# Kernel optimization log

Measured on AMD Instinct MI355X. Metric: run time of the kernel, lower is better.

The kernel has to match this reference:

```python
import jax, jax.numpy as jnp
import numpy as np

H, D, BS = 32, 128, 16  # num heads, head dim, paged-KV block size
ROPE_BASE = 10000.0
NEG_INF = -1e30


def setup_inputs() -> dict:
    key = jax.random.key(0)
    ks = jax.random.split(key, 8)
    B, KV, hidden = 8, 2048, H * D  # decode: one new token per sequence
    max_blocks = KV // BS
    num_slots = B * KV

    hidden_states = jax.random.normal(ks[0], (B, hidden), jnp.float32) * 0.02

    # rotary cos/sin for the current position of each sequence (pos = KV-1)
    inv_freq = 1.0 / (ROPE_BASE ** (jnp.arange(0, D, 2, dtype=jnp.float32) / D))
    pos = jnp.full((B,), KV - 1, jnp.float32)
    ang = pos[:, None] * inv_freq[None, :]            # [B, D/2]
    cos, sin = jnp.cos(ang), jnp.sin(ang)

    w_qkv = jax.random.normal(ks[1], (3 * H * D, hidden), jnp.float32) * 0.02
    b_qkv = jax.random.normal(ks[2], (3 * H * D,), jnp.float32) * 0.02
    w_o = jax.random.normal(ks[3], (hidden, H * D), jnp.float32) * 0.02

    k_cache = jax.random.normal(ks[4], (num_slots, H, D), jnp.float32) * 0.5
    v_cache = jax.random.normal(ks[5], (num_slots, H, D), jnp.float32) * 0.5

    # contiguous block allocation: seq b owns blocks [b*max_blocks, (b+1)*max_blocks)
    block_tables = jnp.arange(B * max_blocks, dtype=jnp.int32).reshape(B, max_blocks)
    slots = (jnp.arange(B, dtype=jnp.int32) * KV + (KV - 1)).astype(jnp.int32)
    input_lengths = jnp.full((B,), KV, jnp.int32)

    return dict(hidden_states=hidden_states, cos=cos, sin=sin,
                w_qkv=w_qkv, b_qkv=b_qkv, w_o=w_o,
                k_cache=k_cache, v_cache=v_cache,
                block_tables=block_tables, slots=slots,
                input_lengths=input_lengths, max_s=KV)


def _rope(x, cos, sin):
    # flash-attn style (non-interleaved) rotary: split head dim in halves
    x1, x2 = jnp.split(x, 2, axis=-1)                 # [T, H, D/2] each
    c, s = cos[:, None, :], sin[:, None, :]
    return jnp.concatenate([x1 * c - x2 * s, x1 * s + x2 * c], axis=-1)


def reference(hidden_states, cos, sin, w_qkv, b_qkv, w_o,
              k_cache, v_cache, block_tables, slots, input_lengths, max_s):
    B = hidden_states.shape[0]
    # fused QKV projection (c_attn, bias=True)
    qkv = hidden_states @ w_qkv.T + b_qkv             # [B, 3*H*D]
    q, k, v = jnp.split(qkv, 3, axis=1)
    q = q.reshape(B, H, D)
    k = k.reshape(B, H, D)
    v = v.reshape(B, H, D)

    # rotary applied in-place to q and k[:,0] in the original
    q = _rope(q, cos, sin)
    k = _rope(k, cos, sin)

    # reshape_and_cache: scatter current k/v into the paged KV cache
    k_cache = k_cache.at[slots].set(k)
    v_cache = v_cache.at[slots].set(v)

    # paged_attn: gather KV via block tables, masked softmax over valid length
    pos = jnp.arange(max_s)                           # [S]
    idx = block_tables[:, pos // BS] * BS + (pos % BS)[None, :]  # [B, S] slot ids
    keys = k_cache[idx]                               # [B, S, H, D]
    vals = v_cache[idx]                               # [B, S, H, D]

    scale = D ** -0.5
    scores = jnp.einsum('bhd,bshd->bhs', q, keys) * scale
    valid = pos[None, :] < input_lengths[:, None]     # [B, S]
    scores = jnp.where(valid[:, None, :], scores, NEG_INF)
    probs = jax.nn.softmax(scores, axis=-1)
    attn = jnp.einsum('bhs,bshd->bhd', probs, vals)   # [B, H, D]

    # o_proj (c_proj, bias=False)
    return attn.reshape(B, H * D) @ w_o.T
```

## Files before the change

kernel.cpp:

```cpp
#include <hip/hip_runtime.h>

#define NH 32
#define HD 128
#define PBS 16
#define HIDDEN (NH * HD)
#define QKVN (3 * HIDDEN)
#define NSPLIT 8
#define KC 512

template <int NR>
__global__ __launch_bounds__(256) void gemv_lds(const float* __restrict__ x,
                                                const float* __restrict__ W,
                                                const float* __restrict__ bias,
                                                float* __restrict__ out,
                                                int N, int K) {
    __shared__ float xs[8][KC];
    const int tid  = threadIdx.x;
    const int lane = tid & 63;
    const int wid  = tid >> 6;
    const int n0   = blockIdx.x * (NR * 4) + wid * NR;
    const float* w0 = W + (size_t)n0 * K;

    float acc[NR][8];
#pragma unroll
    for (int r = 0; r < NR; ++r)
#pragma unroll
        for (int b = 0; b < 8; ++b) acc[r][b] = 0.f;

    for (int kc = 0; kc < K; kc += KC) {
        __syncthreads();
        {
            const int bq  = tid >> 5;
            const int t32 = tid & 31;
            const float* xb = x + (size_t)bq * K + kc;
#pragma unroll
            for (int j = 0; j < 4; ++j) {
                const int off = (t32 + j * 32) * 4;
                *reinterpret_cast<float4*>(&xs[bq][off]) =
                    *reinterpret_cast<const float4*>(xb + off);
            }
        }
        __syncthreads();
#pragma unroll
        for (int j = 0; j < 2; ++j) {
            const int kk = lane * 4 + j * 256;
            float4 w4[NR];
#pragma unroll
            for (int r = 0; r < NR; ++r)
                w4[r] = *reinterpret_cast<const float4*>(w0 + (size_t)r * K + kc + kk);
#pragma unroll
            for (int b = 0; b < 8; ++b) {
                const float4 x4 = *reinterpret_cast<const float4*>(&xs[b][kk]);
#pragma unroll
                for (int r = 0; r < NR; ++r)
                    acc[r][b] += w4[r].x * x4.x + w4[r].y * x4.y +
                                 w4[r].z * x4.z + w4[r].w * x4.w;
            }
        }
    }
#pragma unroll
    for (int r = 0; r < NR; ++r)
#pragma unroll
        for (int b = 0; b < 8; ++b)
#pragma unroll
            for (int off = 32; off > 0; off >>= 1)
                acc[r][b] += __shfl_xor(acc[r][b], off, 64);
    if (lane == 0) {
#pragma unroll
        for (int r = 0; r < NR; ++r) {
            const float bv = bias ? bias[n0 + r] : 0.f;
#pragma unroll
            for (int b = 0; b < 8; ++b)
                out[(size_t)b * N + n0 + r] = acc[r][b] + bv;
        }
    }
}

__global__ __launch_bounds__(256) void rope_k(float* __restrict__ qkv,
                                              const float* __restrict__ cosb,
                                              const float* __restrict__ sinb,
                                              int B) {
    const int tid = blockIdx.x * blockDim.x + threadIdx.x;
    const int total = 2 * B * NH * (HD / 2);
    if (tid >= total) return;
    const int d = tid % (HD / 2);
    const int h = (tid / (HD / 2)) % NH;
    const int b = (tid / (HD / 2) / NH) % B;
    const int part = tid / (HD / 2) / NH / B;
    const float c = cosb[b * (HD / 2) + d];
    const float s = sinb[b * (HD / 2) + d];
    float* p = qkv + (size_t)b * QKVN + part * HIDDEN + h * HD + d;
    const float x1 = p[0];
    const float x2 = p[HD / 2];
    p[0]      = x1 * c - x2 * s;
    p[HD / 2] = x1 * s + x2 * c;
}

__global__ __launch_bounds__(256) void attn_part(const float* __restrict__ qkv,
                                                 const float* __restrict__ k_cache,
                                                 const float* __restrict__ v_cache,
                                                 const int* __restrict__ block_tables,
                                                 const int* __restrict__ slots,
                                                 const int* __restrict__ lengths,
                                                 float* __restrict__ part_o,
                                                 float* __restrict__ part_ml,
                                                 int S, int max_blocks) {
    const int split = blockIdx.x % NSPLIT;
    const int bh    = blockIdx.x / NSPLIT;
    const int b     = bh >> 5;
    const int h     = bh & 31;
    const int SP    = S / NSPLIT;
    const int base  = split * SP;

    __shared__ int   bt[64];
    __shared__ float stage[4][HD + 2];

    const int tid  = threadIdx.x;
    const int lane = tid & 63;
    const int wid  = tid >> 6;
    const int nw   = 4;
    const int half = lane >> 5;
    const int l32  = lane & 31;

    const int nbt = SP / PBS;
    for (int i = tid; i < nbt; i += blockDim.x)
        bt[i] = block_tables[b * max_blocks + base / PBS + i];
    __syncthreads();

    const int slot_b = slots[b];
    const int len    = lengths[b];
    const float scale = 0.088388347648318447f;

    const float* qp   = qkv + (size_t)b * QKVN + h * HD;
    const float* newk = qp + HIDDEN;
    const float* newv = qp + 2 * HIDDEN;
    const float4 q4 = *reinterpret_cast<const float4*>(qp + l32 * 4);

    float m = -1e30f, l = 0.f;
    float4 acc[8];
#pragma unroll
    for (int u = 0; u < 8; ++u) acc[u] = make_float4(0.f, 0.f, 0.f, 0.f);

    const int STEP = nw * 16;
    for (int s0 = wid * 16; s0 < SP; s0 += STEP) {
        float4 k4[8], v4[8];
#pragma unroll
        for (int u = 0; u < 8; ++u) {
            const int p = s0 + u * 2 + half;
            const int idx = bt[p >> 4] * PBS + (p & (PBS - 1));
            const float* kp = (idx == slot_b) ? newk
                                              : (k_cache + (size_t)idx * HIDDEN + h * HD);
            k4[u] = *reinterpret_cast<const float4*>(kp + l32 * 4);
            const float* vp = (idx == slot_b) ? newv
                                              : (v_cache + (size_t)idx * HIDDEN + h * HD);
            v4[u] = *reinterpret_cast<const float4*>(vp + l32 * 4);
        }
        float sc[8];
#pragma unroll
        for (int u = 0; u < 8; ++u) {
            float d = k4[u].x * q4.x + k4[u].y * q4.y + k4[u].z * q4.z + k4[u].w * q4.w;
#pragma unroll
            for (int off = 16; off > 0; off >>= 1) d += __shfl_xor(d, off, 64);
            const int p = s0 + u * 2 + half;
            sc[u] = (base + p < len) ? d * scale : -1e30f;
        }
        float pm = sc[0];
#pragma unroll
        for (int u = 1; u < 8; ++u) pm = fmaxf(pm, sc[u]);
        const float mn = fmaxf(m, pm);
        const float r = __expf(m - mn);
        m = mn;
        l *= r;
        float pu[8];
#pragma unroll
        for (int u = 0; u < 8; ++u) {
            pu[u] = __expf(sc[u] - mn);
            l += pu[u];
        }
#pragma unroll
        for (int u = 0; u < 8; ++u) {
            acc[u].x = fmaf(pu[u], v4[u].x, acc[u].x * r);
            acc[u].y = fmaf(pu[u], v4[u].y, acc[u].y * r);
            acc[u].z = fmaf(pu[u], v4[u].z, acc[u].z * r);
            acc[u].w = fmaf(pu[u], v4[u].w, acc[u].w * r);
        }
    }
    float4 a = acc[0];
#pragma unroll
    for (int u = 1; u < 8; ++u) {
        a.x += acc[u].x; a.y += acc[u].y; a.z += acc[u].z; a.w += acc[u].w;
    }
    {
        const float m2 = __shfl_xor(m, 32, 64);
        const float l2 = __shfl_xor(l, 32, 64);
        float4 a2;
        a2.x = __shfl_xor(a.x, 32, 64);
        a2.y = __shfl_xor(a.y, 32, 64);
        a2.z = __shfl_xor(a.z, 32, 64);
        a2.w = __shfl_xor(a.w, 32, 64);
        const float M  = fmaxf(m, m2);
        const float e1 = __expf(m - M);
        const float e2 = __expf(m2 - M);
        l = l * e1 + l2 * e2;
        a.x = a.x * e1 + a2.x * e2;
        a.y = a.y * e1 + a2.y * e2;
        a.z = a.z * e1 + a2.z * e2;
        a.w = a.w * e1 + a2.w * e2;
        m = M;
    }
    if (half == 0) {
        *reinterpret_cast<float4*>(&stage[wid][l32 * 4]) = a;
        if (l32 == 0) { stage[wid][HD] = m; stage[wid][HD + 1] = l; }
    }
    __syncthreads();
    if (wid == 0) {
        float M4 = stage[0][HD];
#pragma unroll
        for (int w = 1; w < 4; ++w) M4 = fmaxf(M4, stage[w][HD]);
        float L = 0.f, t0 = 0.f, t1 = 0.f;
#pragma unroll
        for (int w = 0; w < 4; ++w) {
            const float e = __expf(stage[w][HD] - M4);
            L  += stage[w][HD + 1] * e;
            t0 += stage[w][lane * 2] * e;
            t1 += stage[w][lane * 2 + 1] * e;
        }
        float* po = part_o + ((size_t)bh * NSPLIT + split) * HD;
        po[lane * 2]     = t0;
        po[lane * 2 + 1] = t1;
        if (lane == 0) {
            part_ml[((size_t)bh * NSPLIT + split) * 2]     = M4;
            part_ml[((size_t)bh * NSPLIT + split) * 2 + 1] = L;
        }
    }
}

__global__ __launch_bounds__(HD) void attn_reduce(const float* __restrict__ part_o,
                                                  const float* __restrict__ part_ml,
                                                  float* __restrict__ attn_out) {
    const int bh = blockIdx.x;
    const int d  = threadIdx.x;
    float M = -1e30f;
#pragma unroll
    for (int i = 0; i < NSPLIT; ++i)
        M = fmaxf(M, part_ml[((size_t)bh * NSPLIT + i) * 2]);
    float L = 0.f, o = 0.f;
#pragma unroll
    for (int i = 0; i < NSPLIT; ++i) {
        const float mi = part_ml[((size_t)bh * NSPLIT + i) * 2];
        const float li = part_ml[((size_t)bh * NSPLIT + i) * 2 + 1];
        const float w  = __expf(mi - M);
        L += li * w;
        o += part_o[((size_t)bh * NSPLIT + i) * HD + d] * w;
    }
    attn_out[(size_t)bh * HD + d] = o / L;
}

extern "C" void kernel_launch(void* const* d_in, const int* in_sizes, int n_in,
                              void* d_out, int out_size, void* d_ws, size_t ws_size,
                              hipStream_t stream) {
    const float* hidden  = (const float*)d_in[0];
    const float* cosb    = (const float*)d_in[1];
    const float* sinb    = (const float*)d_in[2];
    const float* w_qkv   = (const float*)d_in[3];
    const float* b_qkv   = (const float*)d_in[4];
    const float* w_o     = (const float*)d_in[5];
    const float* k_cache = (const float*)d_in[6];
    const float* v_cache = (const float*)d_in[7];
    const int*   btab    = (const int*)d_in[8];
    const int*   slots   = (const int*)d_in[9];
    const int*   lens    = (const int*)d_in[10];

    const int B = in_sizes[0] / HIDDEN;
    const int max_blocks = in_sizes[8] / B;
    const int S = max_blocks * PBS;

    float* qkv     = (float*)d_ws;
    float* attn    = qkv + (size_t)B * QKVN;
    float* part_o  = attn + (size_t)B * HIDDEN;
    float* part_ml = part_o + (size_t)B * NH * NSPLIT * HD;
    float* out     = (float*)d_out;

    gemv_lds<4><<<QKVN / 16, 256, 0, stream>>>(hidden, w_qkv, b_qkv, qkv, QKVN, HIDDEN);

    {
        const int total = 2 * B * NH * (HD / 2);
        rope_k<<<(total + 255) / 256, 256, 0, stream>>>(qkv, cosb, sinb, B);
    }

    attn_part<<<B * NH * NSPLIT, 256, 0, stream>>>(qkv, k_cache, v_cache,
                                                   btab, slots, lens,
                                                   part_o, part_ml, S, max_blocks);
    attn_reduce<<<B * NH, HD, 0, stream>>>(part_o, part_ml, attn);

    gemv_lds<2><<<HIDDEN / 8, 256, 0, stream>>>(attn, w_o, nullptr, out, HIDDEN, HIDDEN);
}
```

Before: 184.4 us.

## Double-buffer GEMV activation tiles and fuse RoPE into attention kernel

The GEMV kernel now double-buffers the activation chunk in LDS, prefetching the next K-chunk while computing the current one, and issues both halves of the weight loads up front. The separate RoPE kernel is removed: attention blocks rotate q and the new k in registers using a lane shuffle, with cos/sin loaded directly. The goal is fewer barriers per chunk, more weight loads in flight, and one less kernel launch plus a global round-trip. In exchange the GEMV uses twice the shared memory and holds more registers, and every split block recomputes the rotation.

Measured after the change: 201.5 us. 1.09x slower.

```diff
diff --git a/kernel.cpp b/kernel.cpp
--- a/kernel.cpp
+++ b/kernel.cpp
@@ -9,54 +9,73 @@
 #define KC 512
 
 template <int NR>
-__global__ __launch_bounds__(256) void gemv_lds(const float* __restrict__ x,
-                                                const float* __restrict__ W,
-                                                const float* __restrict__ bias,
-                                                float* __restrict__ out,
-                                                int N, int K) {
-    __shared__ float xs[8][KC];
+__global__ __launch_bounds__(256) void gemv_db(const float* __restrict__ x,
+                                               const float* __restrict__ W,
+                                               const float* __restrict__ bias,
+                                               float* __restrict__ out,
+                                               int N, int K) {
+    __shared__ float xs[2][8][KC];
     const int tid  = threadIdx.x;
     const int lane = tid & 63;
     const int wid  = tid >> 6;
     const int n0   = blockIdx.x * (NR * 4) + wid * NR;
     const float* w0 = W + (size_t)n0 * K;
-
+    const int bq  = tid >> 5;
+    const int t32 = tid & 31;
+
+    {
+        const float* xb = x + (size_t)bq * K;
+#pragma unroll
+        for (int j = 0; j < 4; ++j) {
+            const int off = (t32 + j * 32) * 4;
+            *reinterpret_cast<float4*>(&xs[0][bq][off]) =
+                *reinterpret_cast<const float4*>(xb + off);
+        }
+    }
     float acc[NR][8];
 #pragma unroll
     for (int r = 0; r < NR; ++r)
 #pragma unroll
         for (int b = 0; b < 8; ++b) acc[r][b] = 0.f;
 
+    __syncthreads();
+    int cur = 0;
     for (int kc = 0; kc < K; kc += KC) {
-        __syncthreads();
-        {
-            const int bq  = tid >> 5;
-            const int t32 = tid & 31;
-            const float* xb = x + (size_t)bq * K + kc;
+        if (kc + KC < K) {
+            const float* xb = x + (size_t)bq * K + kc + KC;
 #pragma unroll
             for (int j = 0; j < 4; ++j) {
                 const int off = (t32 + j * 32) * 4;
-                *reinterpret_cast<float4*>(&xs[bq][off]) =
+                *reinterpret_cast<float4*>(&xs[cur ^ 1][bq][off]) =
                     *reinterpret_cast<const float4*>(xb + off);
             }
         }
+        const int kk0 = lane * 4;
+        float4 w4a[NR], w4b[NR];
+#pragma unroll
+        for (int r = 0; r < NR; ++r)
+            w4a[r] = *reinterpret_cast<const float4*>(w0 + (size_t)r * K + kc + kk0);
+#pragma unroll
+        for (int r = 0; r < NR; ++r)
+            w4b[r] = *reinterpret_cast<const float4*>(w0 + (size_t)r * K + kc + kk0 + 256);
+#pragma unroll
+        for (int b = 0; b < 8; ++b) {
+            const float4 x4 = *reinterpret_cast<const float4*>(&xs[cur][b][kk0]);
+#pragma unroll
+            for (int r = 0; r < NR; ++r)
+                acc[r][b] += w4a[r].x * x4.x + w4a[r].y * x4.y +
+                             w4a[r].z * x4.z + w4a[r].w * x4.w;
+        }
+#pragma unroll
+        for (int b = 0; b < 8; ++b) {
+            const float4 x4 = *reinterpret_cast<const float4*>(&xs[cur][b][kk0 + 256]);
+#pragma unroll
+            for (int r = 0; r < NR; ++r)
+                acc[r][b] += w4b[r].x * x4.x + w4b[r].y * x4.y +
+                             w4b[r].z * x4.z + w4b[r].w * x4.w;
+        }
         __syncthreads();
-#pragma unroll
-        for (int j = 0; j < 2; ++j) {
-            const int kk = lane * 4 + j * 256;
-            float4 w4[NR];
-#pragma unroll
-            for (int r = 0; r < NR; ++r)
-                w4[r] = *reinterpret_cast<const float4*>(w0 + (size_t)r * K + kc + kk);
-#pragma unroll
-            for (int b = 0; b < 8; ++b) {
-                const float4 x4 = *reinterpret_cast<const float4*>(&xs[b][kk]);
-#pragma unroll
-                for (int r = 0; r < NR; ++r)
-                    acc[r][b] += w4[r].x * x4.x + w4[r].y * x4.y +
-                                 w4[r].z * x4.z + w4[r].w * x4.w;
-            }
-        }
+        cur ^= 1;
     }
 #pragma unroll
     for (int r = 0; r < NR; ++r)
@@ -76,27 +95,9 @@
     }
 }
 
-__global__ __launch_bounds__(256) void rope_k(float* __restrict__ qkv,
-                                              const float* __restrict__ cosb,
-                                              const float* __restrict__ sinb,
-                                              int B) {
-    const int tid = blockIdx.x * blockDim.x + threadIdx.x;
-    const int total = 2 * B * NH * (HD / 2);
-    if (tid >= total) return;
-    const int d = tid % (HD / 2);
-    const int h = (tid / (HD / 2)) % NH;
-    const int b = (tid / (HD / 2) / NH) % B;
-    const int part = tid / (HD / 2) / NH / B;
-    const float c = cosb[b * (HD / 2) + d];
-    const float s = sinb[b * (HD / 2) + d];
-    float* p = qkv + (size_t)b * QKVN + part * HIDDEN + h * HD + d;
-    const float x1 = p[0];
-    const float x2 = p[HD / 2];
-    p[0]      = x1 * c - x2 * s;
-    p[HD / 2] = x1 * s + x2 * c;
-}
-
 __global__ __launch_bounds__(256) void attn_part(const float* __restrict__ qkv,
+                                                 const float* __restrict__ cosb,
+                                                 const float* __restrict__ sinb,
                                                  const float* __restrict__ k_cache,
                                                  const float* __restrict__ v_cache,
                                                  const int* __restrict__ block_tables,
@@ -132,9 +133,34 @@
     const float scale = 0.088388347648318447f;
 
     const float* qp   = qkv + (size_t)b * QKVN + h * HD;
-    const float* newk = qp + HIDDEN;
-    const float* newv = qp + 2 * HIDDEN;
-    const float4 q4 = *reinterpret_cast<const float4*>(qp + l32 * 4);
+    const float* newkp = qp + HIDDEN;
+    const float* newvp = qp + 2 * HIDDEN;
+
+    float4 q4 = *reinterpret_cast<const float4*>(qp + l32 * 4);
+    float4 kn4 = *reinterpret_cast<const float4*>(newkp + l32 * 4);
+    {
+        const float4 c4 = *reinterpret_cast<const float4*>(cosb + b * 64 + (l32 & 15) * 4);
+        const float4 s4 = *reinterpret_cast<const float4*>(sinb + b * 64 + (l32 & 15) * 4);
+        const float sgn = (l32 < 16) ? -1.f : 1.f;
+        float4 qpr, kpr;
+        qpr.x = __shfl_xor(q4.x, 16, 64);
+        qpr.y = __shfl_xor(q4.y, 16, 64);
+        qpr.z = __shfl_xor(q4.z, 16, 64);
+        qpr.w = __shfl_xor(q4.w, 16, 64);
+        kpr.x = __shfl_xor(kn4.x, 16, 64);
+        kpr.y = __shfl_xor(kn4.y, 16, 64);
+        kpr.z = __shfl_xor(kn4.z, 16, 64);
+        kpr.w = __shfl_xor(kn4.w, 16, 64);
+        q4.x = q4.x * c4.x + sgn * qpr.x * s4.x;
+        q4.y = q4.y * c4.y + sgn * qpr.y * s4.y;
+        q4.z = q4.z * c4.z + sgn * qpr.z * s4.z;
+        q4.w = q4.w * c4.w + sgn * qpr.w * s4.w;
+        kn4.x = kn4.x * c4.x + sgn * kpr.x * s4.x;
+        kn4.y = kn4.y * c4.y + sgn * kpr.y * s4.y;
+        kn4.z = kn4.z * c4.z + sgn * kpr.z * s4.z;
+        kn4.w = kn4.w * c4.w + sgn * kpr.w * s4.w;
+    }
+    const float4 nv4 = *reinterpret_cast<const float4*>(newvp + l32 * 4);
 
     float m = -1e30f, l = 0.f;
     float4 acc[8];
@@ -148,12 +174,11 @@
         for (int u = 0; u < 8; ++u) {
             const int p = s0 + u * 2 + half;
             const int idx = bt[p >> 4] * PBS + (p & (PBS - 1));
-            const float* kp = (idx == slot_b) ? newk
-                                              : (k_cache + (size_t)idx * HIDDEN + h * HD);
-            k4[u] = *reinterpret_cast<const float4*>(kp + l32 * 4);
-            const float* vp = (idx == slot_b) ? newv
-                                              : (v_cache + (size_t)idx * HIDDEN + h * HD);
-            v4[u] = *reinterpret_cast<const float4*>(vp + l32 * 4);
+            const bool fresh = (idx == slot_b);
+            const float* kp = k_cache + (size_t)idx * HIDDEN + h * HD;
+            const float* vp = v_cache + (size_t)idx * HIDDEN + h * HD;
+            k4[u] = fresh ? kn4 : *reinterpret_cast<const float4*>(kp + l32 * 4);
+            v4[u] = fresh ? nv4 : *reinterpret_cast<const float4*>(vp + l32 * 4);
         }
         float sc[8];
 #pragma unroll
@@ -281,17 +306,12 @@
     float* part_ml = part_o + (size_t)B * NH * NSPLIT * HD;
     float* out     = (float*)d_out;
 
-    gemv_lds<4><<<QKVN / 16, 256, 0, stream>>>(hidden, w_qkv, b_qkv, qkv, QKVN, HIDDEN);
-
-    {
-        const int total = 2 * B * NH * (HD / 2);
-        rope_k<<<(total + 255) / 256, 256, 0, stream>>>(qkv, cosb, sinb, B);
-    }
-
-    attn_part<<<B * NH * NSPLIT, 256, 0, stream>>>(qkv, k_cache, v_cache,
+    gemv_db<4><<<QKVN / 16, 256, 0, stream>>>(hidden, w_qkv, b_qkv, qkv, QKVN, HIDDEN);
+
+    attn_part<<<B * NH * NSPLIT, 256, 0, stream>>>(qkv, cosb, sinb, k_cache, v_cache,
                                                    btab, slots, lens,
                                                    part_o, part_ml, S, max_blocks);
     attn_reduce<<<B * NH, HD, 0, stream>>>(part_o, part_ml, attn);
 
-    gemv_lds<2><<<HIDDEN / 8, 256, 0, stream>>>(attn, w_o, nullptr, out, HIDDEN, HIDDEN);
+    gemv_db<2><<<HIDDEN / 8, 256, 0, stream>>>(attn, w_o, nullptr, out, HIDDEN, HIDDEN);
 }
```

## Restructure paged attention so each block streams full KV rows for all heads

Applied to the files above, without the earlier changes.

Splits the attention work by (batch, sequence chunk) instead of (batch, head, split). Each 512-thread block handles all 32 heads, with 16 threads per head, so every cache row (all heads contiguous) is read as one contiguous 16 KB span. This targets the strided per-head gather of the old layout and the extra intra-block combine through shared memory. In exchange it adds per-token serial online softmax with shuffles and 64 partial chunks per head, which enlarges the reduce kernel's partial buffers.

Measured after the change: 191.6 us. +3.9%, slower.

```diff
diff --git a/kernel.cpp b/kernel.cpp
--- a/kernel.cpp
+++ b/kernel.cpp
@@ -5,7 +5,7 @@
 #define PBS 16
 #define HIDDEN (NH * HD)
 #define QKVN (3 * HIDDEN)
-#define NSPLIT 8
+#define NCH 64
 #define KC 512
 
 template <int NR>
@@ -96,7 +96,7 @@
     p[HD / 2] = x1 * s + x2 * c;
 }
 
-__global__ __launch_bounds__(256) void attn_part(const float* __restrict__ qkv,
+__global__ __launch_bounds__(512) void attn_rows(const float* __restrict__ qkv,
                                                  const float* __restrict__ k_cache,
                                                  const float* __restrict__ v_cache,
                                                  const int* __restrict__ block_tables,
@@ -105,133 +105,74 @@
                                                  float* __restrict__ part_o,
                                                  float* __restrict__ part_ml,
                                                  int S, int max_blocks) {
-    const int split = blockIdx.x % NSPLIT;
-    const int bh    = blockIdx.x / NSPLIT;
-    const int b     = bh >> 5;
-    const int h     = bh & 31;
-    const int SP    = S / NSPLIT;
-    const int base  = split * SP;
-
-    __shared__ int   bt[64];
-    __shared__ float stage[4][HD + 2];
-
-    const int tid  = threadIdx.x;
-    const int lane = tid & 63;
-    const int wid  = tid >> 6;
-    const int nw   = 4;
-    const int half = lane >> 5;
-    const int l32  = lane & 31;
-
-    const int nbt = SP / PBS;
-    for (int i = tid; i < nbt; i += blockDim.x)
-        bt[i] = block_tables[b * max_blocks + base / PBS + i];
+    const int chunk = blockIdx.x % NCH;
+    const int b     = blockIdx.x / NCH;
+    const int SCH   = S / NCH;
+    const int base  = chunk * SCH;
+
+    __shared__ int bt[8];
+    const int tid = threadIdx.x;
+    if (tid < SCH / PBS)
+        bt[tid] = block_tables[b * max_blocks + base / PBS + tid];
     __syncthreads();
 
+    const int h   = tid >> 4;
+    const int t16 = tid & 15;
     const int slot_b = slots[b];
     const int len    = lengths[b];
     const float scale = 0.088388347648318447f;
 
-    const float* qp   = qkv + (size_t)b * QKVN + h * HD;
-    const float* newk = qp + HIDDEN;
-    const float* newv = qp + 2 * HIDDEN;
-    const float4 q4 = *reinterpret_cast<const float4*>(qp + l32 * 4);
+    const float* qp = qkv + (size_t)b * QKVN + h * HD + t16 * 8;
+    const float4 qa = *reinterpret_cast<const float4*>(qp);
+    const float4 qb = *reinterpret_cast<const float4*>(qp + 4);
+    const float* newk = qkv + (size_t)b * QKVN + HIDDEN;
+    const float* newv = qkv + (size_t)b * QKVN + 2 * HIDDEN;
+    const int doff = h * HD + t16 * 8;
 
     float m = -1e30f, l = 0.f;
-    float4 acc[8];
-#pragma unroll
-    for (int u = 0; u < 8; ++u) acc[u] = make_float4(0.f, 0.f, 0.f, 0.f);
-
-    const int STEP = nw * 16;
-    for (int s0 = wid * 16; s0 < SP; s0 += STEP) {
-        float4 k4[8], v4[8];
-#pragma unroll
-        for (int u = 0; u < 8; ++u) {
-            const int p = s0 + u * 2 + half;
-            const int idx = bt[p >> 4] * PBS + (p & (PBS - 1));
-            const float* kp = (idx == slot_b) ? newk
-                                              : (k_cache + (size_t)idx * HIDDEN + h * HD);
-            k4[u] = *reinterpret_cast<const float4*>(kp + l32 * 4);
-            const float* vp = (idx == slot_b) ? newv
-                                              : (v_cache + (size_t)idx * HIDDEN + h * HD);
-            v4[u] = *reinterpret_cast<const float4*>(vp + l32 * 4);
-        }
-        float sc[8];
-#pragma unroll
-        for (int u = 0; u < 8; ++u) {
-            float d = k4[u].x * q4.x + k4[u].y * q4.y + k4[u].z * q4.z + k4[u].w * q4.w;
-#pragma unroll
-            for (int off = 16; off > 0; off >>= 1) d += __shfl_xor(d, off, 64);
-            const int p = s0 + u * 2 + half;
-            sc[u] = (base + p < len) ? d * scale : -1e30f;
-        }
-        float pm = sc[0];
-#pragma unroll
-        for (int u = 1; u < 8; ++u) pm = fmaxf(pm, sc[u]);
-        const float mn = fmaxf(m, pm);
-        const float r = __expf(m - mn);
+    float4 aa = make_float4(0.f, 0.f, 0.f, 0.f);
+    float4 ab = make_float4(0.f, 0.f, 0.f, 0.f);
+
+#pragma unroll 2
+    for (int s = 0; s < SCH; ++s) {
+        const int p   = base + s;
+        const int idx = bt[s >> 4] * PBS + (p & (PBS - 1));
+        const bool fresh = (idx == slot_b);
+        const float* kr = fresh ? newk : (k_cache + (size_t)idx * HIDDEN);
+        const float* vr = fresh ? newv : (v_cache + (size_t)idx * HIDDEN);
+        const float4 k0 = *reinterpret_cast<const float4*>(kr + doff);
+        const float4 k1 = *reinterpret_cast<const float4*>(kr + doff + 4);
+        const float4 v0 = *reinterpret_cast<const float4*>(vr + doff);
+        const float4 v1 = *reinterpret_cast<const float4*>(vr + doff + 4);
+
+        float d = k0.x * qa.x + k0.y * qa.y + k0.z * qa.z + k0.w * qa.w
+                + k1.x * qb.x + k1.y * qb.y + k1.z * qb.z + k1.w * qb.w;
+#pragma unroll
+        for (int off = 1; off < 16; off <<= 1) d += __shfl_xor(d, off, 64);
+        d *= scale;
+
+        const bool valid = (p < len);
+        const float mn = valid ? fmaxf(m, d) : m;
+        const float r  = __expf(m - mn);
+        const float e  = valid ? __expf(d - mn) : 0.f;
         m = mn;
-        l *= r;
-        float pu[8];
-#pragma unroll
-        for (int u = 0; u < 8; ++u) {
-            pu[u] = __expf(sc[u] - mn);
-            l += pu[u];
-        }
-#pragma unroll
-        for (int u = 0; u < 8; ++u) {
-            acc[u].x = fmaf(pu[u], v4[u].x, acc[u].x * r);
-            acc[u].y = fmaf(pu[u], v4[u].y, acc[u].y * r);
-            acc[u].z = fmaf(pu[u], v4[u].z, acc[u].z * r);
-            acc[u].w = fmaf(pu[u], v4[u].w, acc[u].w * r);
-        }
-    }
-    float4 a = acc[0];
-#pragma unroll
-    for (int u = 1; u < 8; ++u) {
-        a.x += acc[u].x; a.y += acc[u].y; a.z += acc[u].z; a.w += acc[u].w;
-    }
-    {
-        const float m2 = __shfl_xor(m, 32, 64);
-        const float l2 = __shfl_xor(l, 32, 64);
-        float4 a2;
-        a2.x = __shfl_xor(a.x, 32, 64);
-        a2.y = __shfl_xor(a.y, 32, 64);
-        a2.z = __shfl_xor(a.z, 32, 64);
-        a2.w = __shfl_xor(a.w, 32, 64);
-        const float M  = fmaxf(m, m2);
-        const float e1 = __expf(m - M);
-        const float e2 = __expf(m2 - M);
-        l = l * e1 + l2 * e2;
-        a.x = a.x * e1 + a2.x * e2;
-        a.y = a.y * e1 + a2.y * e2;
-        a.z = a.z * e1 + a2.z * e2;
-        a.w = a.w * e1 + a2.w * e2;
-        m = M;
-    }
-    if (half == 0) {
-        *reinterpret_cast<float4*>(&stage[wid][l32 * 4]) = a;
-        if (l32 == 0) { stage[wid][HD] = m; stage[wid][HD + 1] = l; }
-    }
-    __syncthreads();
-    if (wid == 0) {
-        float M4 = stage[0][HD];
-#pragma unroll
-        for (int w = 1; w < 4; ++w) M4 = fmaxf(M4, stage[w][HD]);
-        float L = 0.f, t0 = 0.f, t1 = 0.f;
-#pragma unroll
-        for (int w = 0; w < 4; ++w) {
-            const float e = __expf(stage[w][HD] - M4);
-            L  += stage[w][HD + 1] * e;
-            t0 += stage[w][lane * 2] * e;
-            t1 += stage[w][lane * 2 + 1] * e;
-        }
-        float* po = part_o + ((size_t)bh * NSPLIT + split) * HD;
-        po[lane * 2]     = t0;
-        po[lane * 2 + 1] = t1;
-        if (lane == 0) {
-            part_ml[((size_t)bh * NSPLIT + split) * 2]     = M4;
-            part_ml[((size_t)bh * NSPLIT + split) * 2 + 1] = L;
-        }
+        l = l * r + e;
+        aa.x = fmaf(e, v0.x, aa.x * r);
+        aa.y = fmaf(e, v0.y, aa.y * r);
+        aa.z = fmaf(e, v0.z, aa.z * r);
+        aa.w = fmaf(e, v0.w, aa.w * r);
+        ab.x = fmaf(e, v1.x, ab.x * r);
+        ab.y = fmaf(e, v1.y, ab.y * r);
+        ab.z = fmaf(e, v1.z, ab.z * r);
+        ab.w = fmaf(e, v1.w, ab.w * r);
+    }
+
+    float* po = part_o + ((size_t)(b * NH + h) * NCH + chunk) * HD + t16 * 8;
+    *reinterpret_cast<float4*>(po)     = aa;
+    *reinterpret_cast<float4*>(po + 4) = ab;
+    if (t16 == 0) {
+        part_ml[((size_t)(b * NH + h) * NCH + chunk) * 2]     = m;
+        part_ml[((size_t)(b * NH + h) * NCH + chunk) * 2 + 1] = l;
     }
 }
 
@@ -241,17 +182,17 @@
     const int bh = blockIdx.x;
     const int d  = threadIdx.x;
     float M = -1e30f;
-#pragma unroll
-    for (int i = 0; i < NSPLIT; ++i)
-        M = fmaxf(M, part_ml[((size_t)bh * NSPLIT + i) * 2]);
+#pragma unroll 8
+    for (int i = 0; i < NCH; ++i)
+        M = fmaxf(M, part_ml[((size_t)bh * NCH + i) * 2]);
     float L = 0.f, o = 0.f;
-#pragma unroll
-    for (int i = 0; i < NSPLIT; ++i) {
-        const float mi = part_ml[((size_t)bh * NSPLIT + i) * 2];
-        const float li = part_ml[((size_t)bh * NSPLIT + i) * 2 + 1];
+#pragma unroll 8
+    for (int i = 0; i < NCH; ++i) {
+        const float mi = part_ml[((size_t)bh * NCH + i) * 2];
+        const float li = part_ml[((size_t)bh * NCH + i) * 2 + 1];
         const float w  = __expf(mi - M);
         L += li * w;
-        o += part_o[((size_t)bh * NSPLIT + i) * HD + d] * w;
+        o += part_o[((size_t)bh * NCH + i) * HD + d] * w;
     }
     attn_out[(size_t)bh * HD + d] = o / L;
 }
@@ -278,7 +219,7 @@
     float* qkv     = (float*)d_ws;
     float* attn    = qkv + (size_t)B * QKVN;
     float* part_o  = attn + (size_t)B * HIDDEN;
-    float* part_ml = part_o + (size_t)B * NH * NSPLIT * HD;
+    float* part_ml = part_o + (size_t)B * NH * NCH * HD;
     float* out     = (float*)d_out;
 
     gemv_lds<4><<<QKVN / 16, 256, 0, stream>>>(hidden, w_qkv, b_qkv, qkv, QKVN, HIDDEN);
@@ -288,9 +229,8 @@
         rope_k<<<(total + 255) / 256, 256, 0, stream>>>(qkv, cosb, sinb, B);
     }
 
-    attn_part<<<B * NH * NSPLIT, 256, 0, stream>>>(qkv, k_cache, v_cache,
-                                                   btab, slots, lens,
-                                                   part_o, part_ml, S, max_blocks);
+    attn_rows<<<B * NCH, 512, 0, stream>>>(qkv, k_cache, v_cache, btab, slots,
+                                           lens, part_o, part_ml, S, max_blocks);
     attn_reduce<<<B * NH, HD, 0, stream>>>(part_o, part_ml, attn);
 
     gemv_lds<2><<<HIDDEN / 8, 256, 0, stream>>>(attn, w_o, nullptr, out, HIDDEN, HIDDEN);
```

## Fuse all decode attention stages into one cooperative persistent kernel

Applied to the files above, without the earlier changes.

Replaces the five separate launches (QKV GEMV, RoPE, split attention, split reduce, output GEMV) with a single cooperative kernel of 1024 blocks that uses grid-wide syncs between stages. If the cooperative launch fails it falls back to the old multi-kernel path. The aim is to remove launch gaps and tail effects between stages. The cost is four grid barriers, and every stage is forced to fit a fixed grid and tiling (3 QKV rows per wave, 2 attention units per block). The batch size is hardcoded to 8.

After: 633.1 us. 3.43x slower.

```diff
diff --git a/kernel.cpp b/kernel.cpp
--- a/kernel.cpp
+++ b/kernel.cpp
@@ -1,4 +1,7 @@
 #include <hip/hip_runtime.h>
+#include <hip/hip_cooperative_groups.h>
+
+namespace cg = cooperative_groups;
 
 #define NH 32
 #define HD 128
@@ -7,6 +10,307 @@
 #define QKVN (3 * HIDDEN)
 #define NSPLIT 8
 #define KC 512
+#define GRID 1024
+#define TPB 256
+
+__global__ __launch_bounds__(TPB, 4) void fused_all(
+    const float* __restrict__ hid,
+    const float* __restrict__ cosb, const float* __restrict__ sinb,
+    const float* __restrict__ w_qkv, const float* __restrict__ b_qkv,
+    const float* __restrict__ w_o,
+    const float* __restrict__ k_cache, const float* __restrict__ v_cache,
+    const int* __restrict__ btab, const int* __restrict__ slots,
+    const int* __restrict__ lens,
+    float* __restrict__ qkv, float* __restrict__ attn,
+    float* __restrict__ part_o, float* __restrict__ part_ml,
+    float* __restrict__ out, int S, int max_blocks)
+{
+    cg::grid_group gg = cg::this_grid();
+    __shared__ float smem[8 * KC];
+    const int tid  = threadIdx.x;
+    const int lane = tid & 63;
+    const int wid  = tid >> 6;
+    const int bid  = blockIdx.x;
+    const int bq   = tid >> 5;
+    const int t32  = tid & 31;
+
+    {
+        float (*xs)[KC] = reinterpret_cast<float (*)[KC]>(smem);
+        const int n0 = bid * 12 + wid * 3;
+        const float* w0 = w_qkv + (size_t)n0 * HIDDEN;
+        float acc[3][8];
+#pragma unroll
+        for (int r = 0; r < 3; ++r)
+#pragma unroll
+            for (int b = 0; b < 8; ++b) acc[r][b] = 0.f;
+
+        for (int kc = 0; kc < HIDDEN; kc += KC) {
+            __syncthreads();
+            const float* xb = hid + (size_t)bq * HIDDEN + kc;
+#pragma unroll
+            for (int j = 0; j < 4; ++j) {
+                const int off = (t32 + j * 32) * 4;
+                *reinterpret_cast<float4*>(&xs[bq][off]) =
+                    *reinterpret_cast<const float4*>(xb + off);
+            }
+            __syncthreads();
+#pragma unroll
+            for (int j = 0; j < 2; ++j) {
+                const int kk = lane * 4 + j * 256;
+                float4 w4[3];
+#pragma unroll
+                for (int r = 0; r < 3; ++r)
+                    w4[r] = *reinterpret_cast<const float4*>(w0 + (size_t)r * HIDDEN + kc + kk);
+#pragma unroll
+                for (int b = 0; b < 8; ++b) {
+                    const float4 x4 = *reinterpret_cast<const float4*>(&xs[b][kk]);
+#pragma unroll
+                    for (int r = 0; r < 3; ++r)
+                        acc[r][b] += w4[r].x * x4.x + w4[r].y * x4.y +
+                                     w4[r].z * x4.z + w4[r].w * x4.w;
+                }
+            }
+        }
+#pragma unroll
+        for (int r = 0; r < 3; ++r)
+#pragma unroll
+            for (int b = 0; b < 8; ++b)
+#pragma unroll
+                for (int off = 32; off > 0; off >>= 1)
+                    acc[r][b] += __shfl_xor(acc[r][b], off, 64);
+        if (lane == 0) {
+#pragma unroll
+            for (int r = 0; r < 3; ++r) {
+                const float bv = b_qkv[n0 + r];
+#pragma unroll
+                for (int b = 0; b < 8; ++b)
+                    qkv[(size_t)b * QKVN + n0 + r] = acc[r][b] + bv;
+            }
+        }
+    }
+    gg.sync();
+
+    {
+        const int g = bid * TPB + tid;
+        const int total = 2 * 8 * NH * (HD / 2);
+        if (g < total) {
+            const int d = g % (HD / 2);
+            const int h = (g / (HD / 2)) % NH;
+            const int b = (g / (HD / 2) / NH) % 8;
+            const int part = g / (HD / 2) / NH / 8;
+            const float c = cosb[b * (HD / 2) + d];
+            const float s = sinb[b * (HD / 2) + d];
+            float* p = qkv + (size_t)b * QKVN + part * HIDDEN + h * HD + d;
+            const float x1 = p[0];
+            const float x2 = p[HD / 2];
+            p[0]      = x1 * c - x2 * s;
+            p[HD / 2] = x1 * s + x2 * c;
+        }
+    }
+    gg.sync();
+
+    {
+        float (*stg)[HD + 2] = reinterpret_cast<float (*)[HD + 2]>(smem);
+        int* bt = reinterpret_cast<int*>(smem + 544);
+        const int SP   = S / NSPLIT;
+        const int half = lane >> 5;
+        const int l32  = lane & 31;
+        const float scale = 0.088388347648318447f;
+
+        for (int un = 0; un < 2; ++un) {
+            const int unit  = bid * 2 + un;
+            const int split = unit % NSPLIT;
+            const int bh    = unit / NSPLIT;
+            const int b     = bh >> 5;
+            const int h     = bh & 31;
+            const int base  = split * SP;
+
+            __syncthreads();
+            for (int i = tid; i < SP / PBS; i += TPB)
+                bt[i] = btab[b * max_blocks + base / PBS + i];
+            __syncthreads();
+
+            const int slot_b = slots[b];
+            const int len    = lens[b];
+            const float* qp   = qkv + (size_t)b * QKVN + h * HD;
+            const float* newk = qp + HIDDEN;
+            const float* newv = qp + 2 * HIDDEN;
+            const float4 q4 = *reinterpret_cast<const float4*>(qp + l32 * 4);
+
+            float m = -1e30f, l = 0.f;
+            float4 acc[8];
+#pragma unroll
+            for (int u = 0; u < 8; ++u) acc[u] = make_float4(0.f, 0.f, 0.f, 0.f);
+
+            for (int s0 = wid * 16; s0 < SP; s0 += 64) {
+                int idxs[8];
+                float d8[8];
+                {
+                    float4 k4[8];
+#pragma unroll
+                    for (int u = 0; u < 8; ++u) {
+                        const int p = s0 + u * 2 + half;
+                        idxs[u] = bt[p >> 4] * PBS + (p & (PBS - 1));
+                        k4[u] = (idxs[u] == slot_b)
+                                  ? *reinterpret_cast<const float4*>(newk + l32 * 4)
+                                  : *reinterpret_cast<const float4*>(
+                                        k_cache + (size_t)idxs[u] * HIDDEN + h * HD + l32 * 4);
+                    }
+#pragma unroll
+                    for (int u = 0; u < 8; ++u)
+                        d8[u] = k4[u].x * q4.x + k4[u].y * q4.y +
+                                k4[u].z * q4.z + k4[u].w * q4.w;
+                }
+                float4 v4[8];
+#pragma unroll
+                for (int u = 0; u < 8; ++u)
+                    v4[u] = (idxs[u] == slot_b)
+                              ? *reinterpret_cast<const float4*>(newv + l32 * 4)
+                              : *reinterpret_cast<const float4*>(
+                                    v_cache + (size_t)idxs[u] * HIDDEN + h * HD + l32 * 4);
+                float sc[8];
+#pragma unroll
+                for (int u = 0; u < 8; ++u) {
+                    float d = d8[u];
+#pragma unroll
+                    for (int off = 16; off > 0; off >>= 1) d += __shfl_xor(d, off, 64);
+                    const int p = s0 + u * 2 + half;
+                    sc[u] = (base + p < len) ? d * scale : -1e30f;
+                }
+                float pm = sc[0];
+#pragma unroll
+                for (int u = 1; u < 8; ++u) pm = fmaxf(pm, sc[u]);
+                const float mn = fmaxf(m, pm);
+                const float r = __expf(m - mn);
+                m = mn;
+                l *= r;
+                float pu[8];
+#pragma unroll
+                for (int u = 0; u < 8; ++u) {
+                    pu[u] = __expf(sc[u] - mn);
+                    l += pu[u];
+                }
+#pragma unroll
+                for (int u = 0; u < 8; ++u) {
+                    acc[u].x = fmaf(pu[u], v4[u].x, acc[u].x * r);
+                    acc[u].y = fmaf(pu[u], v4[u].y, acc[u].y * r);
+                    acc[u].z = fmaf(pu[u], v4[u].z, acc[u].z * r);
+                    acc[u].w = fmaf(pu[u], v4[u].w, acc[u].w * r);
+                }
+            }
+            float4 a = acc[0];
+#pragma unroll
+            for (int u = 1; u < 8; ++u) {
+                a.x += acc[u].x; a.y += acc[u].y; a.z += acc[u].z; a.w += acc[u].w;
+            }
+            {
+                const float m2 = __shfl_xor(m, 32, 64);
+                const float l2 = __shfl_xor(l, 32, 64);
+                float4 a2;
+                a2.x = __shfl_xor(a.x, 32, 64);
+                a2.y = __shfl_xor(a.y, 32, 64);
+                a2.z = __shfl_xor(a.z, 32, 64);
+                a2.w = __shfl_xor(a.w, 32, 64);
+                const float M  = fmaxf(m, m2);
+                const float e1 = __expf(m - M);
+                const float e2 = __expf(m2 - M);
+                l = l * e1 + l2 * e2;
+                a.x = a.x * e1 + a2.x * e2;
+                a.y = a.y * e1 + a2.y * e2;
+                a.z = a.z * e1 + a2.z * e2;
+                a.w = a.w * e1 + a2.w * e2;
+                m = M;
+            }
+            if (half == 0) {
+                *reinterpret_cast<float4*>(&stg[wid][l32 * 4]) = a;
+                if (l32 == 0) { stg[wid][HD] = m; stg[wid][HD + 1] = l; }
+            }
+            __syncthreads();
+            if (wid == 0) {
+                float M4 = stg[0][HD];
+#pragma unroll
+                for (int w = 1; w < 4; ++w) M4 = fmaxf(M4, stg[w][HD]);
+                float L = 0.f, t0 = 0.f, t1 = 0.f;
+#pragma unroll
+                for (int w = 0; w < 4; ++w) {
+                    const float e = __expf(stg[w][HD] - M4);
+                    L  += stg[w][HD + 1] * e;
+                    t0 += stg[w][lane * 2] * e;
+                    t1 += stg[w][lane * 2 + 1] * e;
+                }
+                float* po = part_o + ((size_t)bh * NSPLIT + split) * HD;
+                po[lane * 2]     = t0;
+                po[lane * 2 + 1] = t1;
+                if (lane == 0) {
+                    part_ml[((size_t)bh * NSPLIT + split) * 2]     = M4;
+                    part_ml[((size_t)bh * NSPLIT + split) * 2 + 1] = L;
+                }
+            }
+        }
+    }
+    gg.sync();
+
+    if (bid < 8 * NH && tid < HD) {
+        const int bh = bid;
+        const int d  = tid;
+        float M = -1e30f;
+#pragma unroll
+        for (int i = 0; i < NSPLIT; ++i)
+            M = fmaxf(M, part_ml[((size_t)bh * NSPLIT + i) * 2]);
+        float L = 0.f, o = 0.f;
+#pragma unroll
+        for (int i = 0; i < NSPLIT; ++i) {
+            const float mi = part_ml[((size_t)bh * NSPLIT + i) * 2];
+            const float li = part_ml[((size_t)bh * NSPLIT + i) * 2 + 1];
+            const float w  = __expf(mi - M);
+            L += li * w;
+            o += part_o[((size_t)bh * NSPLIT + i) * HD + d] * w;
+        }
+        attn[(size_t)bh * HD + d] = o / L;
+    }
+    gg.sync();
+
+    {
+        float (*xs)[KC] = reinterpret_cast<float (*)[KC]>(smem);
+        const int n0 = bid * 4 + wid;
+        const float* w0 = w_o + (size_t)n0 * HIDDEN;
+        float acc[8];
+#pragma unroll
+        for (int b = 0; b < 8; ++b) acc[b] = 0.f;
+
+        for (int kc = 0; kc < HIDDEN; kc += KC) {
+            __syncthreads();
+            const float* xb = attn + (size_t)bq * HIDDEN + kc;
+#pragma unroll
+            for (int j = 0; j < 4; ++j) {
+                const int off = (t32 + j * 32) * 4;
+                *reinterpret_cast<float4*>(&xs[bq][off]) =
+                    *reinterpret_cast<const float4*>(xb + off);
+            }
+            __syncthreads();
+#pragma unroll
+            for (int j = 0; j < 2; ++j) {
+                const int kk = lane * 4 + j * 256;
+                const float4 w4 = *reinterpret_cast<const float4*>(w0 + kc + kk);
+#pragma unroll
+                for (int b = 0; b < 8; ++b) {
+                    const float4 x4 = *reinterpret_cast<const float4*>(&xs[b][kk]);
+                    acc[b] += w4.x * x4.x + w4.y * x4.y + w4.z * x4.z + w4.w * x4.w;
+                }
+            }
+        }
+#pragma unroll
+        for (int b = 0; b < 8; ++b)
+#pragma unroll
+            for (int off = 32; off > 0; off >>= 1)
+                acc[b] += __shfl_xor(acc[b], off, 64);
+        if (lane == 0) {
+#pragma unroll
+            for (int b = 0; b < 8; ++b)
+                out[(size_t)b * HIDDEN + n0] = acc[b];
+        }
+    }
+}
 
 template <int NR>
 __global__ __launch_bounds__(256) void gemv_lds(const float* __restrict__ x,
@@ -96,15 +400,15 @@
     p[HD / 2] = x1 * s + x2 * c;
 }
 
-__global__ __launch_bounds__(256) void attn_part(const float* __restrict__ qkv,
-                                                 const float* __restrict__ k_cache,
-                                                 const float* __restrict__ v_cache,
-                                                 const int* __restrict__ block_tables,
-                                                 const int* __restrict__ slots,
-                                                 const int* __restrict__ lengths,
-                                                 float* __restrict__ part_o,
-                                                 float* __restrict__ part_ml,
-                                                 int S, int max_blocks) {
+__global__ __launch_bounds__(256) void attn_part_fb(const float* __restrict__ qkv,
+                                                    const float* __restrict__ k_cache,
+                                                    const float* __restrict__ v_cache,
+                                                    const int* __restrict__ block_tables,
+                                                    const int* __restrict__ slots,
+                                                    const int* __restrict__ lengths,
+                                                    float* __restrict__ part_o,
+                                                    float* __restrict__ part_ml,
+                                                    int S, int max_blocks) {
     const int split = blockIdx.x % NSPLIT;
     const int bh    = blockIdx.x / NSPLIT;
     const int b     = bh >> 5;
@@ -118,12 +422,10 @@
     const int tid  = threadIdx.x;
     const int lane = tid & 63;
     const int wid  = tid >> 6;
-    const int nw   = 4;
     const int half = lane >> 5;
     const int l32  = lane & 31;
 
-    const int nbt = SP / PBS;
-    for (int i = tid; i < nbt; i += blockDim.x)
+    for (int i = tid; i < SP / PBS; i += blockDim.x)
         bt[i] = block_tables[b * max_blocks + base / PBS + i];
     __syncthreads();
 
@@ -141,19 +443,19 @@
 #pragma unroll
     for (int u = 0; u < 8; ++u) acc[u] = make_float4(0.f, 0.f, 0.f, 0.f);
 
-    const int STEP = nw * 16;
-    for (int s0 = wid * 16; s0 < SP; s0 += STEP) {
+    for (int s0 = wid * 16; s0 < SP; s0 += 64) {
         float4 k4[8], v4[8];
 #pragma unroll
         for (int u = 0; u < 8; ++u) {
             const int p = s0 + u * 2 + half;
             const int idx = bt[p >> 4] * PBS + (p & (PBS - 1));
-            const float* kp = (idx == slot_b) ? newk
-                                              : (k_cache + (size_t)idx * HIDDEN + h * HD);
-            k4[u] = *reinterpret_cast<const float4*>(kp + l32 * 4);
-            const float* vp = (idx == slot_b) ? newv
-                                              : (v_cache + (size_t)idx * HIDDEN + h * HD);
-            v4[u] = *reinterpret_cast<const float4*>(vp + l32 * 4);
+            const bool fresh = (idx == slot_b);
+            k4[u] = fresh ? *reinterpret_cast<const float4*>(newk + l32 * 4)
+                          : *reinterpret_cast<const float4*>(
+                                k_cache + (size_t)idx * HIDDEN + h * HD + l32 * 4);
+            v4[u] = fresh ? *reinterpret_cast<const float4*>(newv + l32 * 4)
+                          : *reinterpret_cast<const float4*>(
+                                v_cache + (size_t)idx * HIDDEN + h * HD + l32 * 4);
         }
         float sc[8];
 #pragma unroll
@@ -259,7 +561,7 @@
 extern "C" void kernel_launch(void* const* d_in, const int* in_sizes, int n_in,
                               void* d_out, int out_size, void* d_ws, size_t ws_size,
                               hipStream_t stream) {
-    const float* hidden  = (const float*)d_in[0];
+    const float* hid     = (const float*)d_in[0];
     const float* cosb    = (const float*)d_in[1];
     const float* sinb    = (const float*)d_in[2];
     const float* w_qkv   = (const float*)d_in[3];
@@ -272,8 +574,8 @@
     const int*   lens    = (const int*)d_in[10];
 
     const int B = in_sizes[0] / HIDDEN;
-    const int max_blocks = in_sizes[8] / B;
-    const int S = max_blocks * PBS;
+    int max_blocks = in_sizes[8] / B;
+    int S = max_blocks * PBS;
 
     float* qkv     = (float*)d_ws;
     float* attn    = qkv + (size_t)B * QKVN;
@@ -281,17 +583,22 @@
     float* part_ml = part_o + (size_t)B * NH * NSPLIT * HD;
     float* out     = (float*)d_out;
 
-    gemv_lds<4><<<QKVN / 16, 256, 0, stream>>>(hidden, w_qkv, b_qkv, qkv, QKVN, HIDDEN);
-
-    {
+    void* args[] = {
+        (void*)&hid, (void*)&cosb, (void*)&sinb, (void*)&w_qkv, (void*)&b_qkv,
+        (void*)&w_o, (void*)&k_cache, (void*)&v_cache, (void*)&btab,
+        (void*)&slots, (void*)&lens, (void*)&qkv, (void*)&attn,
+        (void*)&part_o, (void*)&part_ml, (void*)&out, (void*)&S, (void*)&max_blocks
+    };
+    hipError_t err = hipLaunchCooperativeKernel((void*)fused_all, dim3(GRID),
+                                                dim3(TPB), args, 0, stream);
+    if (err != hipSuccess) {
+        gemv_lds<4><<<QKVN / 16, 256, 0, stream>>>(hid, w_qkv, b_qkv, qkv, QKVN, HIDDEN);
         const int total = 2 * B * NH * (HD / 2);
         rope_k<<<(total + 255) / 256, 256, 0, stream>>>(qkv, cosb, sinb, B);
-    }
-
-    attn_part<<<B * NH * NSPLIT, 256, 0, stream>>>(qkv, k_cache, v_cache,
-                                                   btab, slots, lens,
-                                                   part_o, part_ml, S, max_blocks);
-    attn_reduce<<<B * NH, HD, 0, stream>>>(part_o, part_ml, attn);
-
-    gemv_lds<2><<<HIDDEN / 8, 256, 0, stream>>>(attn, w_o, nullptr, out, HIDDEN, HIDDEN);
+        attn_part_fb<<<B * NH * NSPLIT, 256, 0, stream>>>(qkv, k_cache, v_cache,
+                                                          btab, slots, lens,
+                                                          part_o, part_ml, S, max_blocks);
+        attn_reduce<<<B * NH, HD, 0, stream>>>(part_o, part_ml, attn);
+        gemv_lds<2><<<HIDDEN / 8, 256, 0, stream>>>(attn, w_o, nullptr, out, HIDDEN, HIDDEN);
+    }
 }
```
